# Optimization experiments

Measured on AMD Instinct MI355X. Metric: run time of the kernel, lower is better.

Reference implementation:

```python
import jax, jax.numpy as jnp
import numpy as np

HEADS = 16
DIM_HEAD = 64
SCALE = DIM_HEAD ** -0.5
STEP = 0.6

def setup_inputs() -> dict:
    key = jax.random.key(0)
    ks = jax.random.split(key, 8)
    B, N, QD = 2, 2048, 1024
    M, CD = 1024, 768
    inner = HEADS * DIM_HEAD  # 1024
    return {
        "x": jax.random.normal(ks[0], (B, N, QD), jnp.float32),
        "context": jax.random.normal(ks[1], (B, M, CD), jnp.float32),
        "focused_attention_mask": jax.random.uniform(ks[2], (1, M, M), jnp.float32),
        "Wq": jax.random.normal(ks[3], (inner, QD), jnp.float32) * 0.02,
        "Wk": jax.random.normal(ks[4], (inner, CD), jnp.float32) * 0.02,
        "Wv": jax.random.normal(ks[5], (inner, CD), jnp.float32) * 0.02,
        "Wo": jax.random.normal(ks[6], (QD, inner), jnp.float32) * 0.02,
        "bo": jax.random.normal(ks[7], (QD,), jnp.float32) * 0.02,
    }

def _split_heads(t, h):
    b, n, hd = t.shape
    return t.reshape(b, n, h, hd // h).transpose(0, 2, 1, 3).reshape(b * h, n, hd // h)

def reference(x, context, focused_attention_mask, Wq, Wk, Wv, Wo, bo):
    b, n, _ = x.shape
    h = HEADS
    q = _split_heads(x @ Wq.T, h)        # (b h) n d
    k = _split_heads(context @ Wk.T, h)  # (b h) m d
    v = _split_heads(context @ Wv.T, h)
    sim = jnp.einsum('bid,bjd->bij', q, k) * SCALE  # (b h) n m
    # FCA focus-weight modulation (fam has leading dim 1, broadcast over b*h)
    fam = focused_attention_mask[0]  # (m, m)
    K = fam.shape[-1]
    fw = jnp.abs(jnp.einsum('bqk,dk->bqd', sim[:, :, :K], fam))  # (b h) n m
    fw = jnp.minimum(fw, 1.0)
    fw = fw / (jnp.max(fw, axis=2, keepdims=True) + 1e-6)
    fw = (fw > STEP).astype(sim.dtype)
    sim = sim.at[:, :, :K].add((fw - 1.0) * 50.0)
    attn = jax.nn.softmax(sim, axis=-1)
    out = jnp.einsum('bij,bjd->bid', attn, v)  # (b h) n d
    out = out.reshape(b, h, n, -1).transpose(0, 2, 1, 3).reshape(b, n, -1)
    return out @ Wo.T + bo
```

## Files before the change

kernel.cpp:

```cpp
#include <hip/hip_runtime.h>
#include <hip/hip_fp16.h>
#include <math.h>

#define SCALE 0.125f

typedef _Float16 f16;
typedef __attribute__((ext_vector_type(8))) _Float16 f16x8;
typedef __attribute__((ext_vector_type(4))) float f32x4;

#define MFMA(a, b, c) __builtin_amdgcn_mfma_f32_16x16x32_f16((a), (b), (c), 0, 0, 0)

#define LX(r, qd) (((r) << 6) + ((((qd) ^ ((r) & 7))) << 3))

__device__ __forceinline__ void gll16(const f16* g, f16* l) {
    __builtin_amdgcn_global_load_lds(
        (const __attribute__((address_space(1))) unsigned int*)(g),
        (__attribute__((address_space(3))) unsigned int*)(l),
        16, 0, 0);
}

struct SplitSeg { const float* src; f16* h; f16* l; float scale; size_t n; };
struct SplitArgs { SplitSeg seg[7]; };

__global__ __launch_bounds__(256) void split_all(SplitArgs a)
{
    SplitSeg s = a.seg[blockIdx.y];
    size_t i4 = ((size_t)blockIdx.x * 256 + threadIdx.x) * 4;
    size_t stride = (size_t)gridDim.x * 256 * 4;
    for (; i4 < s.n; i4 += stride) {
        float4 v = *(const float4*)&s.src[i4];
        float av[4] = {v.x * s.scale, v.y * s.scale, v.z * s.scale, v.w * s.scale};
        f16 hv[4], lv[4];
#pragma unroll
        for (int j = 0; j < 4; ++j) {
            hv[j] = (f16)av[j];
            lv[j] = (f16)(av[j] - (float)hv[j]);
        }
        *(float2*)&s.h[i4] = *(float2*)hv;
        *(float2*)&s.l[i4] = *(float2*)lv;
    }
}

template <int AP, int BP>
__global__ __launch_bounds__(256) void gemm16(
    const f16* __restrict__ Ah, const f16* __restrict__ Al, size_t Abat,
    const f16* __restrict__ Bh, const f16* __restrict__ Bl, int Bstr, size_t Bbat,
    float* __restrict__ Cf, const float* __restrict__ bias,
    f16* __restrict__ Ch, f16* __restrict__ Cl, int Cpitch,
    f16* __restrict__ Cth, f16* __restrict__ Ctl, int Mt,
    int Nsplit, f16* __restrict__ C2th, int Mt2,
    size_t Cbat, float oscale, int M, int N, int K)
{
    constexpr int NCH = AP * 16 + BP * 8;
    __shared__ __align__(16) f16 Ash[AP][128 * 64];
    __shared__ __align__(16) f16 Bsh[BP][64 * 64];

    const int tid  = threadIdx.x;
    const int z    = blockIdx.z;
    Ah += z * Abat; if (AP == 2) Al += z * Abat;
    Bh += z * Bbat; if (BP == 2) Bl += z * Bbat;
    const int m0   = blockIdx.y * 128;
    const int n0   = blockIdx.x * 64;
    const int w    = tid >> 6;
    const int lane = tid & 63;
    const int wm   = (w >> 1) * 64;
    const int wn   = (w & 1) * 32;
    const int lq   = lane >> 4;
    const int l15  = lane & 15;
    const int sr   = lane >> 3;
    const int sg   = lane & 7;

    f32x4 acc[4][2];
#pragma unroll
    for (int mi = 0; mi < 4; ++mi)
#pragma unroll
        for (int ni = 0; ni < 2; ++ni) acc[mi][ni] = (f32x4){0.f, 0.f, 0.f, 0.f};

    for (int k0 = 0; k0 < K; k0 += 64) {
        __syncthreads();
#pragma unroll
        for (int c = 0; c < NCH / 4; ++c) {
            int chunk = c * 4 + w;
            const f16* gp; f16* lp;
            if (chunk < AP * 16) {
                int pl = chunk >> 4, sub = chunk & 15;
                int r = sub * 8 + sr;
                int g = sg ^ (r & 7);
                gp = ((AP == 2 && pl) ? Al : Ah) + (size_t)(m0 + r) * K + k0 + g * 8;
                lp = &Ash[pl][sub * 512];
            } else {
                int cb = chunk - AP * 16;
                int pl = cb >> 3, sub = cb & 7;
                int r = sub * 8 + sr;
                int g = sg ^ (r & 7);
                gp = ((BP == 2 && pl) ? Bl : Bh) + (size_t)(n0 + r) * Bstr + k0 + g * 8;
                lp = &Bsh[pl][sub * 512];
            }
            gll16(gp, lp);
        }
        __syncthreads();

#pragma unroll
        for (int kc = 0; kc < 2; ++kc) {
            f16x8 afh[4], afl[4];
#pragma unroll
            for (int mi = 0; mi < 4; ++mi) {
                int r = wm + mi * 16 + l15;
                afh[mi] = *(const f16x8*)&Ash[0][LX(r, kc * 4 + lq)];
                if (AP == 2) afl[mi] = *(const f16x8*)&Ash[1][LX(r, kc * 4 + lq)];
            }
#pragma unroll
            for (int ni = 0; ni < 2; ++ni) {
                int r = wn + ni * 16 + l15;
                f16x8 bh = *(const f16x8*)&Bsh[0][LX(r, kc * 4 + lq)];
                f16x8 bl;
                if (BP == 2) bl = *(const f16x8*)&Bsh[1][LX(r, kc * 4 + lq)];
#pragma unroll
                for (int mi = 0; mi < 4; ++mi) {
                    f32x4 a = acc[mi][ni];
                    a = MFMA(afh[mi], bh, a);
                    if (BP == 2) a = MFMA(afh[mi], bl, a);
                    if (AP == 2) a = MFMA(afl[mi], bh, a);
                    acc[mi][ni] = a;
                }
            }
        }
    }

    const bool vhalf = (Nsplit > 0) && (n0 >= Nsplit);
    if (Cf)  Cf  += z * Cbat;
    if (Ch)  { Ch += z * Cbat; if (Cl) Cl += z * Cbat; }

#pragma unroll
    for (int mi = 0; mi < 4; ++mi) {
#pragma unroll
        for (int ni = 0; ni < 2; ++ni) {
            int row = m0 + wm + mi * 16 + lq * 4;
            int col = n0 + wn + ni * 16 + l15;
            float v[4];
#pragma unroll
            for (int r = 0; r < 4; ++r) v[r] = acc[mi][ni][r] * oscale;
            if (Cf) {
                float bb = bias ? bias[col] : 0.f;
#pragma unroll
                for (int r = 0; r < 4; ++r)
                    Cf[(size_t)(row + r) * Cpitch + col] = v[r] + bb;
            } else if (vhalf) {
                union { f16 a[4]; float2 f; } uh;
#pragma unroll
                for (int r = 0; r < 4; ++r) uh.a[r] = (f16)v[r];
                *(float2*)&C2th[(size_t)(col - Nsplit) * Mt2 + row] = uh.f;
            } else {
                if (Ch) {
#pragma unroll
                    for (int r = 0; r < 4; ++r) {
                        f16 hh = (f16)v[r];
                        Ch[(size_t)(row + r) * Cpitch + col] = hh;
                        if (Cl) Cl[(size_t)(row + r) * Cpitch + col] = (f16)(v[r] - (float)hh);
                    }
                }
                if (Cth) {
                    union { f16 a[4]; float2 f; } uh, ul;
#pragma unroll
                    for (int r = 0; r < 4; ++r) {
                        uh.a[r] = (f16)v[r];
                        ul.a[r] = (f16)(v[r] - (float)uh.a[r]);
                    }
                    *(float2*)&Cth[(size_t)col * Mt + row] = uh.f;
                    if (Ctl) *(float2*)&Ctl[(size_t)col * Mt + row] = ul.f;
                }
            }
        }
    }
}

__global__ __launch_bounds__(256) void attn_mfma(
    const f16* __restrict__ Qh, const f16* __restrict__ Ql,
    const f16* __restrict__ Kh,
    const f16* __restrict__ Gh, const f16* __restrict__ Gl,
    const f16* __restrict__ Vth, f16* __restrict__ AOh)
{
    __shared__ __align__(16) f16 Ksh[2][4096];
    __shared__ __align__(16) f16 Gsh[2][2][4096];
    __shared__ __align__(16) f16 Vsh[4096];
    __shared__ __align__(16) f16 Ps[128 * 72];
    __shared__ int eflag[4];

    const int tid = threadIdx.x;
    const int bh = blockIdx.x;
    const int b = bh >> 4, h = bh & 15;
    const int qr0 = blockIdx.y * 128;
    const int w = tid >> 6, lane = tid & 63;
    const int lq = lane >> 4, l15 = lane & 15;
    const int wq = w * 32;

    const size_t qb = ((size_t)(b * 2048 + qr0)) * 1024 + h * 64;
    const size_t kb = ((size_t)(b * 1024)) * 1024 + h * 64;
    const size_t vb = (size_t)(h * 64) * 2048 + b * 1024;

    const int sr = lane >> 3;
    const int ss = lane & 7;

    f16x8 aqh[2][2], aql[2][2];
#pragma unroll
    for (int ti = 0; ti < 2; ++ti)
#pragma unroll
        for (int kc = 0; kc < 2; ++kc) {
            size_t off = qb + (size_t)(wq + ti * 16 + l15) * 1024 + (kc * 4 + lq) * 8;
            aqh[ti][kc] = *(const f16x8*)&Qh[off];
            aql[ti][kc] = *(const f16x8*)&Ql[off];
        }

    float mx[2][4] = {};
    for (int jt = 0; jt < 16; ++jt) {
#pragma unroll
        for (int c = 0; c < 4; ++c) {
            int chunk = c * 4 + w;
            int pl = chunk >> 3, sub = chunk & 7;
            int r = sub * 8 + sr;
            int g = ss ^ (r & 7);
            const f16* gp = (pl ? Gl : Gh) + kb + (size_t)(jt * 64 + r) * 1024 + g * 8;
            gll16(gp, &Gsh[0][pl][sub * 512]);
        }
        __syncthreads();

#pragma unroll
        for (int tj = 0; tj < 4; ++tj) {
            f32x4 a0 = {0.f, 0.f, 0.f, 0.f}, a1 = {0.f, 0.f, 0.f, 0.f};
#pragma unroll
            for (int kc = 0; kc < 2; ++kc) {
                int lx = LX(tj * 16 + l15, kc * 4 + lq);
                f16x8 bgh = *(const f16x8*)&Gsh[0][0][lx];
                f16x8 bgl = *(const f16x8*)&Gsh[0][1][lx];
                a0 = MFMA(aqh[0][kc], bgh, a0);
                a0 = MFMA(aqh[0][kc], bgl, a0);
                a0 = MFMA(aql[0][kc], bgh, a0);
                a1 = MFMA(aqh[1][kc], bgh, a1);
                a1 = MFMA(aqh[1][kc], bgl, a1);
                a1 = MFMA(aql[1][kc], bgh, a1);
            }
#pragma unroll
            for (int r = 0; r < 4; ++r) {
                mx[0][r] = fmaxf(mx[0][r], fminf(fabsf(a0[r] * SCALE), 1.f));
                mx[1][r] = fmaxf(mx[1][r], fminf(fabsf(a1[r] * SCALE), 1.f));
            }
        }
        bool done = true;
#pragma unroll
        for (int ti = 0; ti < 2; ++ti)
#pragma unroll
            for (int r = 0; r < 4; ++r) {
                float m = mx[ti][r];
#pragma unroll
                for (int d = 1; d < 16; d <<= 1)
                    m = fmaxf(m, __shfl_xor(m, d, 64));
                mx[ti][r] = m;
                done = done && (m >= 1.0f);
            }
        int wd = __all(done ? 1 : 0);
        if (lane == 0) eflag[w] = wd;
        __syncthreads();
        if (eflag[0] && eflag[1] && eflag[2] && eflag[3]) break;
    }
    float T[2][4];
#pragma unroll
    for (int ti = 0; ti < 2; ++ti)
#pragma unroll
        for (int r = 0; r < 4; ++r)
            T[ti][r] = 4.8f * (mx[ti][r] + 1e-6f);

    const float SL2E = 0.125f * 1.44269504088896f;
    const float PEN2 = -50.0f * 1.44269504088896f;
    f32x4 aco[2][4];
#pragma unroll
    for (int ti = 0; ti < 2; ++ti)
#pragma unroll
        for (int dj = 0; dj < 4; ++dj) aco[ti][dj] = (f32x4){0.f, 0.f, 0.f, 0.f};
    float dsum[2][4] = {};

#pragma unroll
    for (int c = 0; c < 6; ++c) {
        int chunk = c * 4 + w;
        int sub = chunk & 7;
        int r = sub * 8 + sr;
        int g = ss ^ (r & 7);
        size_t off = kb + (size_t)r * 1024 + g * 8;
        const f16* gp; f16* lp;
        if (chunk < 8)       { gp = Kh + off; lp = &Ksh[0][sub * 512]; }
        else if (chunk < 16) { gp = Gh + off; lp = &Gsh[0][0][sub * 512]; }
        else                 { gp = Gl + off; lp = &Gsh[0][1][sub * 512]; }
        gll16(gp, lp);
    }

    for (int jt = 0; jt < 16; ++jt) {
        const int cur = jt & 1;

#pragma unroll
        for (int c = 0; c < 2; ++c) {
            int chunk = c * 4 + w;
            int sub = chunk & 7;
            int r = sub * 8 + sr;
            int g = ss ^ (r & 7);
            const f16* gp = Vth + vb + (size_t)r * 2048 + jt * 64 + g * 8;
            gll16(gp, &Vsh[sub * 512]);
        }
        if (jt < 15) {
#pragma unroll
            for (int c = 0; c < 6; ++c) {
                int chunk = c * 4 + w;
                int sub = chunk & 7;
                int r = sub * 8 + sr;
                int g = ss ^ (r & 7);
                size_t off = kb + (size_t)((jt + 1) * 64 + r) * 1024 + g * 8;
                const f16* gp; f16* lp;
                if (chunk < 8)       { gp = Kh + off; lp = &Ksh[cur ^ 1][sub * 512]; }
                else if (chunk < 16) { gp = Gh + off; lp = &Gsh[cur ^ 1][0][sub * 512]; }
                else                 { gp = Gl + off; lp = &Gsh[cur ^ 1][1][sub * 512]; }
                gll16(gp, lp);
            }
            asm volatile("s_waitcnt vmcnt(8)" ::: "memory");
        } else {
            asm volatile("s_waitcnt vmcnt(2)" ::: "memory");
        }
        __builtin_amdgcn_s_barrier();
        __builtin_amdgcn_sched_barrier(0);

#pragma unroll
        for (int tj = 0; tj < 4; ++tj) {
            f32x4 s0 = {0.f, 0.f, 0.f, 0.f}, s1 = {0.f, 0.f, 0.f, 0.f};
            f32x4 f0 = {0.f, 0.f, 0.f, 0.f}, f1 = {0.f, 0.f, 0.f, 0.f};
            __builtin_amdgcn_s_setprio(1);
#pragma unroll
            for (int kc = 0; kc < 2; ++kc) {
                int lx = LX(tj * 16 + l15, kc * 4 + lq);
                f16x8 bkh = *(const f16x8*)&Ksh[cur][lx];
                f16x8 bgh = *(const f16x8*)&Gsh[cur][0][lx];
                f16x8 bgl = *(const f16x8*)&Gsh[cur][1][lx];
                s0 = MFMA(aqh[0][kc], bkh, s0);
                f0 = MFMA(aqh[0][kc], bgh, f0);
                f0 = MFMA(aqh[0][kc], bgl, f0);
                f0 = MFMA(aql[0][kc], bgh, f0);
                s1 = MFMA(aqh[1][kc], bkh, s1);
                f1 = MFMA(aqh[1][kc], bgh, f1);
                f1 = MFMA(aqh[1][kc], bgl, f1);
                f1 = MFMA(aql[1][kc], bgh, f1);
            }
            __builtin_amdgcn_s_setprio(0);
#pragma unroll
            for (int r = 0; r < 4; ++r) {
                float p0 = (fabsf(f0[r]) > T[0][r]) ? 0.f : PEN2;
                f16 e0 = (f16)exp2f(fmaf(s0[r], SL2E, p0));
                Ps[(wq + lq * 4 + r) * 72 + tj * 16 + l15] = e0;
                dsum[0][r] += (float)e0;
                float p1 = (fabsf(f1[r]) > T[1][r]) ? 0.f : PEN2;
                f16 e1 = (f16)exp2f(fmaf(s1[r], SL2E, p1));
                Ps[(wq + 16 + lq * 4 + r) * 72 + tj * 16 + l15] = e1;
                dsum[1][r] += (float)e1;
            }
        }

        if (jt < 15) asm volatile("s_waitcnt vmcnt(6)" ::: "memory");
        else         asm volatile("s_waitcnt vmcnt(0)" ::: "memory");
        asm volatile("s_waitcnt lgkmcnt(0)" ::: "memory");
        __builtin_amdgcn_sched_barrier(0);
        __builtin_amdgcn_s_barrier();
        __builtin_amdgcn_sched_barrier(0);

        __builtin_amdgcn_s_setprio(1);
#pragma unroll
        for (int kc = 0; kc < 2; ++kc) {
            f16x8 ap0 = *(const f16x8*)&Ps[(wq + l15) * 72 + kc * 32 + lq * 8];
            f16x8 ap1 = *(const f16x8*)&Ps[(wq + 16 + l15) * 72 + kc * 32 + lq * 8];
#pragma unroll
            for (int dj = 0; dj < 4; ++dj) {
                int lx = LX(dj * 16 + l15, kc * 4 + lq);
                f16x8 bvh = *(const f16x8*)&Vsh[lx];
                aco[0][dj] = MFMA(ap0, bvh, aco[0][dj]);
                aco[1][dj] = MFMA(ap1, bvh, aco[1][dj]);
            }
        }
        __builtin_amdgcn_s_setprio(0);

        asm volatile("s_waitcnt lgkmcnt(0)" ::: "memory");
        __builtin_amdgcn_sched_barrier(0);
        __builtin_amdgcn_s_barrier();
        __builtin_amdgcn_sched_barrier(0);
    }

#pragma unroll
    for (int ti = 0; ti < 2; ++ti)
#pragma unroll
        for (int r = 0; r < 4; ++r) {
            float s = dsum[ti][r];
#pragma unroll
            for (int d = 1; d < 16; d <<= 1)
                s += __shfl_xor(s, d, 64);
            dsum[ti][r] = s;
        }
#pragma unroll
    for (int ti = 0; ti < 2; ++ti) {
#pragma unroll
        for (int r = 0; r < 4; ++r) {
            float invd = 1.0f / dsum[ti][r];
            int qq = qr0 + wq + ti * 16 + lq * 4 + r;
#pragma unroll
            for (int dj = 0; dj < 4; ++dj) {
                int dd = h * 64 + dj * 16 + l15;
                AOh[(size_t)(b * 2048 + qq) * 1024 + dd] = (f16)(aco[ti][dj][r] * invd);
            }
        }
    }
}

extern "C" void kernel_launch(void* const* d_in, const int* in_sizes, int n_in,
                              void* d_out, int out_size, void* d_ws, size_t ws_size,
                              hipStream_t stream)
{
    const float* x   = (const float*)d_in[0];
    const float* ctx = (const float*)d_in[1];
    const float* fam = (const float*)d_in[2];
    const float* Wq  = (const float*)d_in[3];
    const float* Wk  = (const float*)d_in[4];
    const float* Wv  = (const float*)d_in[5];
    const float* Wo  = (const float*)d_in[6];
    const float* bo  = (const float*)d_in[7];
    float* out = (float*)d_out;

    const size_t nX  = (size_t)4096 * 1024;
    const size_t nC  = (size_t)2048 * 768;
    const size_t nWq = (size_t)1024 * 1024;
    const size_t nWk = (size_t)1024 * 768;
    const size_t nF  = (size_t)1024 * 1024;
    const size_t nK  = (size_t)2048 * 1024;

    char* p = (char*)d_ws;
    f16 *xh   = (f16*)p; p += nX * 2;   f16 *xl   = (f16*)p; p += nX * 2;
    f16 *ch   = (f16*)p; p += nC * 2;   f16 *cl   = (f16*)p; p += nC * 2;
    f16 *wqh  = (f16*)p; p += nWq * 2;  f16 *wql  = (f16*)p; p += nWq * 2;
    f16 *wkvh = (f16*)p; p += nWk * 4;  f16 *wkvl = (f16*)p; p += nWk * 4;
    f16 *woh  = (f16*)p; p += nWq * 2;  f16 *wol  = (f16*)p; p += nWq * 2;
    f16 *fmh  = (f16*)p; p += nF * 2;   f16 *fml  = (f16*)p; p += nF * 2;
    f16 *qh   = (f16*)p; p += nX * 2;   f16 *ql   = (f16*)p; p += nX * 2;
    f16 *kh   = (f16*)p; p += nK * 2;
    f16 *kth  = (f16*)p; p += nK * 2;   f16 *ktl  = (f16*)p; p += nK * 2;
    f16 *vth  = (f16*)p; p += nK * 2;
    f16 *gh   = (f16*)p; p += nK * 2;   f16 *gl   = (f16*)p; p += nK * 2;
    f16 *aoh  = (f16*)p; p += nX * 2;

    const float WS  = 64.0f;
    const float IWS = 1.0f / 64.0f;

    SplitArgs sa;
    sa.seg[0] = {x,   xh,          xl,          1.f, nX};
    sa.seg[1] = {ctx, ch,          cl,          1.f, nC};
    sa.seg[2] = {Wq,  wqh,         wql,         WS,  nWq};
    sa.seg[3] = {Wk,  wkvh,        wkvl,        WS,  nWk};
    sa.seg[4] = {Wv,  wkvh + nWk,  wkvl + nWk,  WS,  nWk};
    sa.seg[5] = {Wo,  woh,         wol,         WS,  nWq};
    sa.seg[6] = {fam, fmh,         fml,         1.f, nF};
    split_all<<<dim3(64, 7), 256, 0, stream>>>(sa);

    gemm16<2, 2><<<dim3(16, 32, 1), 256, 0, stream>>>(
        xh, xl, 0, wqh, wql, 1024, 0,
        nullptr, nullptr, qh, ql, 1024, nullptr, nullptr, 0,
        0, nullptr, 0, 0, IWS, 4096, 1024, 1024);

    gemm16<2, 2><<<dim3(32, 16, 1), 256, 0, stream>>>(
        ch, cl, 0, wkvh, wkvl, 768, 0,
        nullptr, nullptr, kh, nullptr, 1024, kth, ktl, 2048,
        1024, vth, 2048, 0, IWS, 2048, 2048, 768);

    gemm16<2, 2><<<dim3(16, 8, 2), 256, 0, stream>>>(
        fmh, fml, 0, kth, ktl, 2048, 1024,
        nullptr, nullptr, gh, gl, 1024, nullptr, nullptr, 0,
        0, nullptr, 0, (size_t)1024 * 1024, 1.f, 1024, 1024, 1024);

    attn_mfma<<<dim3(32, 16), 256, 0, stream>>>(qh, ql, kh, gh, gl, vth, aoh);

    gemm16<1, 1><<<dim3(16, 32, 1), 256, 0, stream>>>(
        aoh, nullptr, 0, woh, nullptr, 1024, 0,
        out, bo, nullptr, nullptr, 1024, nullptr, nullptr, 0,
        0, nullptr, 0, 0, IWS, 4096, 1024, 1024);
}
```

Before: 278.9 us.

## Shrink attention tiles to 64 queries and load V fragments directly to registers

```diff
diff --git a/kernel.cpp b/kernel.cpp
--- a/kernel.cpp
+++ b/kernel.cpp
@@ -17,6 +17,12 @@
         (const __attribute__((address_space(1))) unsigned int*)(g),
         (__attribute__((address_space(3))) unsigned int*)(l),
         16, 0, 0);
+}
+
+__device__ __forceinline__ f16x8 gload16(const f16* p) {
+    f16x8 r;
+    asm volatile("global_load_dwordx4 %0, %1, off" : "=v"(r) : "v"(p) : "memory");
+    return r;
 }
 
 struct SplitSeg { const float* src; f16* h; f16* l; float scale; size_t n; };
@@ -174,25 +180,24 @@
     }
 }
 
-__global__ __launch_bounds__(256) void attn_mfma(
+__global__ __launch_bounds__(256, 4) void attn_mfma(
     const f16* __restrict__ Qh, const f16* __restrict__ Ql,
     const f16* __restrict__ Kh,
     const f16* __restrict__ Gh, const f16* __restrict__ Gl,
     const f16* __restrict__ Vth, f16* __restrict__ AOh)
 {
-    __shared__ __align__(16) f16 Ksh[2][4096];
-    __shared__ __align__(16) f16 Gsh[2][2][4096];
-    __shared__ __align__(16) f16 Vsh[4096];
-    __shared__ __align__(16) f16 Ps[128 * 72];
+    __shared__ __align__(16) f16 Ksh[2][2048];
+    __shared__ __align__(16) f16 Gsh[2][2][2048];
+    __shared__ __align__(16) f16 Ps[64 * 40];
     __shared__ int eflag[4];
 
     const int tid = threadIdx.x;
     const int bh = blockIdx.x;
     const int b = bh >> 4, h = bh & 15;
-    const int qr0 = blockIdx.y * 128;
+    const int qr0 = blockIdx.y * 64;
     const int w = tid >> 6, lane = tid & 63;
     const int lq = lane >> 4, l15 = lane & 15;
-    const int wq = w * 32;
+    const int wq = w * 16;
 
     const size_t qb = ((size_t)(b * 2048 + qr0)) * 1024 + h * 64;
     const size_t kb = ((size_t)(b * 1024)) * 1024 + h * 64;
@@ -201,134 +206,110 @@
     const int sr = lane >> 3;
     const int ss = lane & 7;
 
-    f16x8 aqh[2][2], aql[2][2];
-#pragma unroll
-    for (int ti = 0; ti < 2; ++ti)
-#pragma unroll
-        for (int kc = 0; kc < 2; ++kc) {
-            size_t off = qb + (size_t)(wq + ti * 16 + l15) * 1024 + (kc * 4 + lq) * 8;
-            aqh[ti][kc] = *(const f16x8*)&Qh[off];
-            aql[ti][kc] = *(const f16x8*)&Ql[off];
-        }
-
-    float mx[2][4] = {};
-    for (int jt = 0; jt < 16; ++jt) {
-#pragma unroll
-        for (int c = 0; c < 4; ++c) {
+    f16x8 aqh[2], aql[2];
+#pragma unroll
+    for (int kc = 0; kc < 2; ++kc) {
+        size_t off = qb + (size_t)(wq + l15) * 1024 + (kc * 4 + lq) * 8;
+        aqh[kc] = *(const f16x8*)&Qh[off];
+        aql[kc] = *(const f16x8*)&Ql[off];
+    }
+
+    float mx[4] = {};
+    for (int jt = 0; jt < 32; ++jt) {
+#pragma unroll
+        for (int c = 0; c < 2; ++c) {
             int chunk = c * 4 + w;
-            int pl = chunk >> 3, sub = chunk & 7;
+            int pl = chunk >> 2, sub = chunk & 3;
             int r = sub * 8 + sr;
             int g = ss ^ (r & 7);
-            const f16* gp = (pl ? Gl : Gh) + kb + (size_t)(jt * 64 + r) * 1024 + g * 8;
+            const f16* gp = (pl ? Gl : Gh) + kb + (size_t)(jt * 32 + r) * 1024 + g * 8;
             gll16(gp, &Gsh[0][pl][sub * 512]);
         }
         __syncthreads();
 
 #pragma unroll
-        for (int tj = 0; tj < 4; ++tj) {
-            f32x4 a0 = {0.f, 0.f, 0.f, 0.f}, a1 = {0.f, 0.f, 0.f, 0.f};
+        for (int tj = 0; tj < 2; ++tj) {
+            f32x4 a0 = {0.f, 0.f, 0.f, 0.f};
 #pragma unroll
             for (int kc = 0; kc < 2; ++kc) {
                 int lx = LX(tj * 16 + l15, kc * 4 + lq);
                 f16x8 bgh = *(const f16x8*)&Gsh[0][0][lx];
                 f16x8 bgl = *(const f16x8*)&Gsh[0][1][lx];
-                a0 = MFMA(aqh[0][kc], bgh, a0);
-                a0 = MFMA(aqh[0][kc], bgl, a0);
-                a0 = MFMA(aql[0][kc], bgh, a0);
-                a1 = MFMA(aqh[1][kc], bgh, a1);
-                a1 = MFMA(aqh[1][kc], bgl, a1);
-                a1 = MFMA(aql[1][kc], bgh, a1);
-            }
-#pragma unroll
-            for (int r = 0; r < 4; ++r) {
-                mx[0][r] = fmaxf(mx[0][r], fminf(fabsf(a0[r] * SCALE), 1.f));
-                mx[1][r] = fmaxf(mx[1][r], fminf(fabsf(a1[r] * SCALE), 1.f));
-            }
+                a0 = MFMA(aqh[kc], bgh, a0);
+                a0 = MFMA(aqh[kc], bgl, a0);
+                a0 = MFMA(aql[kc], bgh, a0);
+            }
+#pragma unroll
+            for (int r = 0; r < 4; ++r)
+                mx[r] = fmaxf(mx[r], fminf(fabsf(a0[r] * SCALE), 1.f));
         }
         bool done = true;
 #pragma unroll
-        for (int ti = 0; ti < 2; ++ti)
-#pragma unroll
-            for (int r = 0; r < 4; ++r) {
-                float m = mx[ti][r];
-#pragma unroll
-                for (int d = 1; d < 16; d <<= 1)
-                    m = fmaxf(m, __shfl_xor(m, d, 64));
-                mx[ti][r] = m;
-                done = done && (m >= 1.0f);
-            }
+        for (int r = 0; r < 4; ++r) {
+            float m = mx[r];
+#pragma unroll
+            for (int d = 1; d < 16; d <<= 1)
+                m = fmaxf(m, __shfl_xor(m, d, 64));
+            mx[r] = m;
+            done = done && (m >= 1.0f);
+        }
         int wd = __all(done ? 1 : 0);
         if (lane == 0) eflag[w] = wd;
         __syncthreads();
         if (eflag[0] && eflag[1] && eflag[2] && eflag[3]) break;
     }
-    float T[2][4];
-#pragma unroll
-    for (int ti = 0; ti < 2; ++ti)
-#pragma unroll
-        for (int r = 0; r < 4; ++r)
-            T[ti][r] = 4.8f * (mx[ti][r] + 1e-6f);
+    float T[4];
+#pragma unroll
+    for (int r = 0; r < 4; ++r)
+        T[r] = 4.8f * (mx[r] + 1e-6f);
 
     const float SL2E = 0.125f * 1.44269504088896f;
     const float PEN2 = -50.0f * 1.44269504088896f;
-    f32x4 aco[2][4];
-#pragma unroll
-    for (int ti = 0; ti < 2; ++ti)
-#pragma unroll
-        for (int dj = 0; dj < 4; ++dj) aco[ti][dj] = (f32x4){0.f, 0.f, 0.f, 0.f};
-    float dsum[2][4] = {};
-
-#pragma unroll
-    for (int c = 0; c < 6; ++c) {
-        int chunk = c * 4 + w;
-        int sub = chunk & 7;
-        int r = sub * 8 + sr;
-        int g = ss ^ (r & 7);
-        size_t off = kb + (size_t)r * 1024 + g * 8;
-        const f16* gp; f16* lp;
-        if (chunk < 8)       { gp = Kh + off; lp = &Ksh[0][sub * 512]; }
-        else if (chunk < 16) { gp = Gh + off; lp = &Gsh[0][0][sub * 512]; }
-        else                 { gp = Gl + off; lp = &Gsh[0][1][sub * 512]; }
-        gll16(gp, lp);
-    }
-
-    for (int jt = 0; jt < 16; ++jt) {
-        const int cur = jt & 1;
-
-#pragma unroll
-        for (int c = 0; c < 2; ++c) {
+    f32x4 aco[4];
+#pragma unroll
+    for (int dj = 0; dj < 4; ++dj) aco[dj] = (f32x4){0.f, 0.f, 0.f, 0.f};
+    float dsum[4] = {};
+
+    auto stageKG = [&](int jtn, int buf) {
+#pragma unroll
+        for (int c = 0; c < 3; ++c) {
             int chunk = c * 4 + w;
-            int sub = chunk & 7;
+            bool isK = chunk < 4;
+            int cb = isK ? chunk : chunk - 4;
+            int pl = isK ? 0 : (cb >> 2);
+            int sub = isK ? cb : (cb & 3);
             int r = sub * 8 + sr;
             int g = ss ^ (r & 7);
-            const f16* gp = Vth + vb + (size_t)r * 2048 + jt * 64 + g * 8;
-            gll16(gp, &Vsh[sub * 512]);
-        }
-        if (jt < 15) {
-#pragma unroll
-            for (int c = 0; c < 6; ++c) {
-                int chunk = c * 4 + w;
-                int sub = chunk & 7;
-                int r = sub * 8 + sr;
-                int g = ss ^ (r & 7);
-                size_t off = kb + (size_t)((jt + 1) * 64 + r) * 1024 + g * 8;
-                const f16* gp; f16* lp;
-                if (chunk < 8)       { gp = Kh + off; lp = &Ksh[cur ^ 1][sub * 512]; }
-                else if (chunk < 16) { gp = Gh + off; lp = &Gsh[cur ^ 1][0][sub * 512]; }
-                else                 { gp = Gl + off; lp = &Gsh[cur ^ 1][1][sub * 512]; }
-                gll16(gp, lp);
-            }
-            asm volatile("s_waitcnt vmcnt(8)" ::: "memory");
+            size_t off = kb + (size_t)(jtn * 32 + r) * 1024 + g * 8;
+            const f16* gp = isK ? (Kh + off) : ((pl ? Gl : Gh) + off);
+            f16* lp = isK ? &Ksh[buf][sub * 512] : &Gsh[buf][pl][sub * 512];
+            gll16(gp, lp);
+        }
+    };
+
+    stageKG(0, 0);
+
+    for (int jt = 0; jt < 32; ++jt) {
+        const int cur = jt & 1;
+
+        f16x8 vf[4];
+#pragma unroll
+        for (int dj = 0; dj < 4; ++dj)
+            vf[dj] = gload16(&Vth[vb + (size_t)(dj * 16 + l15) * 2048 + jt * 32 + lq * 8]);
+
+        if (jt < 31) {
+            stageKG(jt + 1, cur ^ 1);
+            asm volatile("s_waitcnt vmcnt(7)" ::: "memory");
         } else {
-            asm volatile("s_waitcnt vmcnt(2)" ::: "memory");
-        }
+            asm volatile("s_waitcnt vmcnt(4)" ::: "memory");
+        }
+        __builtin_amdgcn_sched_barrier(0);
         __builtin_amdgcn_s_barrier();
         __builtin_amdgcn_sched_barrier(0);
 
 #pragma unroll
-        for (int tj = 0; tj < 4; ++tj) {
-            f32x4 s0 = {0.f, 0.f, 0.f, 0.f}, s1 = {0.f, 0.f, 0.f, 0.f};
-            f32x4 f0 = {0.f, 0.f, 0.f, 0.f}, f1 = {0.f, 0.f, 0.f, 0.f};
+        for (int tj = 0; tj < 2; ++tj) {
+            f32x4 s0 = {0.f, 0.f, 0.f, 0.f}, f0 = {0.f, 0.f, 0.f, 0.f};
             __builtin_amdgcn_s_setprio(1);
 #pragma unroll
             for (int kc = 0; kc < 2; ++kc) {
@@ -336,78 +317,53 @@
                 f16x8 bkh = *(const f16x8*)&Ksh[cur][lx];
                 f16x8 bgh = *(const f16x8*)&Gsh[cur][0][lx];
                 f16x8 bgl = *(const f16x8*)&Gsh[cur][1][lx];
-                s0 = MFMA(aqh[0][kc], bkh, s0);
-                f0 = MFMA(aqh[0][kc], bgh, f0);
-                f0 = MFMA(aqh[0][kc], bgl, f0);
-                f0 = MFMA(aql[0][kc], bgh, f0);
-                s1 = MFMA(aqh[1][kc], bkh, s1);
-                f1 = MFMA(aqh[1][kc], bgh, f1);
-                f1 = MFMA(aqh[1][kc], bgl, f1);
-                f1 = MFMA(aql[1][kc], bgh, f1);
+                s0 = MFMA(aqh[kc], bkh, s0);
+                f0 = MFMA(aqh[kc], bgh, f0);
+                f0 = MFMA(aqh[kc], bgl, f0);
+                f0 = MFMA(aql[kc], bgh, f0);
             }
             __builtin_amdgcn_s_setprio(0);
 #pragma unroll
             for (int r = 0; r < 4; ++r) {
-                float p0 = (fabsf(f0[r]) > T[0][r]) ? 0.f : PEN2;
+                float p0 = (fabsf(f0[r]) > T[r]) ? 0.f : PEN2;
                 f16 e0 = (f16)exp2f(fmaf(s0[r], SL2E, p0));
-                Ps[(wq + lq * 4 + r) * 72 + tj * 16 + l15] = e0;
-                dsum[0][r] += (float)e0;
-                float p1 = (fabsf(f1[r]) > T[1][r]) ? 0.f : PEN2;
-                f16 e1 = (f16)exp2f(fmaf(s1[r], SL2E, p1));
-                Ps[(wq + 16 + lq * 4 + r) * 72 + tj * 16 + l15] = e1;
-                dsum[1][r] += (float)e1;
-            }
-        }
-
-        if (jt < 15) asm volatile("s_waitcnt vmcnt(6)" ::: "memory");
+                Ps[(wq + lq * 4 + r) * 40 + tj * 16 + l15] = e0;
+                dsum[r] += (float)e0;
+            }
+        }
+
+        if (jt < 31) asm volatile("s_waitcnt vmcnt(3)" ::: "memory");
         else         asm volatile("s_waitcnt vmcnt(0)" ::: "memory");
-        asm volatile("s_waitcnt lgkmcnt(0)" ::: "memory");
+        __builtin_amdgcn_sched_barrier(0);
+
+        f16x8 ap = *(const f16x8*)&Ps[(wq + l15) * 40 + lq * 8];
+        __builtin_amdgcn_s_setprio(1);
+#pragma unroll
+        for (int dj = 0; dj < 4; ++dj)
+            aco[dj] = MFMA(ap, vf[dj], aco[dj]);
+        __builtin_amdgcn_s_setprio(0);
+
         __builtin_amdgcn_sched_barrier(0);
         __builtin_amdgcn_s_barrier();
         __builtin_amdgcn_sched_barrier(0);
-
-        __builtin_amdgcn_s_setprio(1);
-#pragma unroll
-        for (int kc = 0; kc < 2; ++kc) {
-            f16x8 ap0 = *(const f16x8*)&Ps[(wq + l15) * 72 + kc * 32 + lq * 8];
-            f16x8 ap1 = *(const f16x8*)&Ps[(wq + 16 + l15) * 72 + kc * 32 + lq * 8];
-#pragma unroll
-            for (int dj = 0; dj < 4; ++dj) {
-                int lx = LX(dj * 16 + l15, kc * 4 + lq);
-                f16x8 bvh = *(const f16x8*)&Vsh[lx];
-                aco[0][dj] = MFMA(ap0, bvh, aco[0][dj]);
-                aco[1][dj] = MFMA(ap1, bvh, aco[1][dj]);
-            }
-        }
-        __builtin_amdgcn_s_setprio(0);
-
-        asm volatile("s_waitcnt lgkmcnt(0)" ::: "memory");
-        __builtin_amdgcn_sched_barrier(0);
-        __builtin_amdgcn_s_barrier();
-        __builtin_amdgcn_sched_barrier(0);
-    }
-
-#pragma unroll
-    for (int ti = 0; ti < 2; ++ti)
-#pragma unroll
-        for (int r = 0; r < 4; ++r) {
-            float s = dsum[ti][r];
-#pragma unroll
-            for (int d = 1; d < 16; d <<= 1)
-                s += __shfl_xor(s, d, 64);
-            dsum[ti][r] = s;
-        }
-#pragma unroll
-    for (int ti = 0; ti < 2; ++ti) {
-#pragma unroll
-        for (int r = 0; r < 4; ++r) {
-            float invd = 1.0f / dsum[ti][r];
-            int qq = qr0 + wq + ti * 16 + lq * 4 + r;
-#pragma unroll
-            for (int dj = 0; dj < 4; ++dj) {
-                int dd = h * 64 + dj * 16 + l15;
-                AOh[(size_t)(b * 2048 + qq) * 1024 + dd] = (f16)(aco[ti][dj][r] * invd);
-            }
+    }
+
+#pragma unroll
+    for (int r = 0; r < 4; ++r) {
+        float s = dsum[r];
+#pragma unroll
+        for (int d = 1; d < 16; d <<= 1)
+            s += __shfl_xor(s, d, 64);
+        dsum[r] = s;
+    }
+#pragma unroll
+    for (int r = 0; r < 4; ++r) {
+        float invd = 1.0f / dsum[r];
+        int qq = qr0 + wq + lq * 4 + r;
+#pragma unroll
+        for (int dj = 0; dj < 4; ++dj) {
+            int dd = h * 64 + dj * 16 + l15;
+            AOh[(size_t)(b * 2048 + qq) * 1024 + dd] = (f16)(aco[dj][r] * invd);
         }
     }
 }
@@ -475,7 +431,7 @@
         nullptr, nullptr, gh, gl, 1024, nullptr, nullptr, 0,
         0, nullptr, 0, (size_t)1024 * 1024, 1.f, 1024, 1024, 1024);
 
-    attn_mfma<<<dim3(32, 16), 256, 0, stream>>>(qh, ql, kh, gh, gl, vth, aoh);
+    attn_mfma<<<dim3(32, 32), 256, 0, stream>>>(qh, ql, kh, gh, gl, vth, aoh);
 
     gemm16<1, 1><<<dim3(16, 32, 1), 256, 0, stream>>>(
         aoh, nullptr, 0, woh, nullptr, 1024, 0,
```

Measured after the change: 353.8 us. 1.27x slower.
